# Optimization experiments

Measured on AMD Instinct MI355X. Metric: run time of the kernel, lower is better.

Reference implementation:

```python
import jax, jax.numpy as jnp
import numpy as np

TOP_K = 2
N_EXPERTS = 64
NEG_INF = -1e30  # stand-in for -inf; only used implicitly via sparse softmax


def setup_inputs() -> dict:
    key = jax.random.key(0)
    k1, k2, k3, k4 = jax.random.split(key, 4)
    n_embd, n_exp = 2048, N_EXPERTS
    B, S = 4, 4096
    scale = 1.0 / np.sqrt(n_embd)
    return {
        "x": jax.random.normal(k1, (B, S, n_embd), dtype=jnp.float32),
        "noise_eps": jax.random.normal(k2, (B, S, n_exp), dtype=jnp.float32),
        "W_route": jax.random.normal(k3, (n_embd, n_exp), dtype=jnp.float32) * scale,
        "b_route": jnp.zeros((n_exp,), dtype=jnp.float32),
        "W_noise": jax.random.normal(k4, (n_embd, n_exp), dtype=jnp.float32) * scale,
        "b_noise": jnp.zeros((n_exp,), dtype=jnp.float32),
    }


def reference(x, noise_eps, W_route, b_route, W_noise, b_noise):
    # r_act, noise_scale: [B, S, E]
    r_act = jnp.einsum("bsd,de->bse", x, W_route) + b_route
    noise_raw = jnp.einsum("bsd,de->bse", x, W_noise) + b_noise
    noisy = r_act + noise_eps * jax.nn.softplus(noise_raw)

    topk_logits, idx = jax.lax.top_k(noisy, TOP_K)  # [B, S, k]
    # softmax over a -inf-filled scatter == softmax over the top-k values,
    # scattered back with zeros elsewhere (exp(-inf) = 0)
    probs_k = jax.nn.softmax(topk_logits, axis=-1)  # [B, S, k]
    one_hot = jax.nn.one_hot(idx, N_EXPERTS, dtype=probs_k.dtype)  # [B, S, k, E]
    r_out = jnp.einsum("bsk,bske->bse", probs_k, one_hot)
    return r_out, idx
```

## Files before the change

### kernel.cpp

```cpp
#include <hip/hip_runtime.h>
#include <math.h>


typedef _Float16 f16;
typedef _Float16 f16x4 __attribute__((ext_vector_type(4)));
typedef _Float16 f16x8 __attribute__((ext_vector_type(8)));
typedef float    f32x4 __attribute__((ext_vector_type(4)));

#define NEMBD 2048
#define NEXP  64
#define BM    64
#define BK    32
#define NCH   (NEMBD / BK)
#define XP    40
#define WP    40
#define WSCALE 64.0f
#define INV_WSCALE 0.015625f

union F4H8 { float4 f; f16x8 h; };

__global__ __launch_bounds__(256) void build_wt(
    const float* __restrict__ Wr, const float* __restrict__ Wn,
    f16* __restrict__ wt_hi, f16* __restrict__ wt_lo)
{
    __shared__ float ws[BK][129];
    const int c = blockIdx.x, t = threadIdx.x;
    const int k0 = c * BK;
    {
        const int k  = t >> 3;
        const int n8 = (t & 7) << 3;
        const float* s0 = Wr + (size_t)(k0 + k) * NEXP + n8;
        const float* s1 = Wn + (size_t)(k0 + k) * NEXP + n8;
        #pragma unroll
        for (int j = 0; j < 8; ++j) ws[k][n8 + j] = s0[j];
        #pragma unroll
        for (int j = 0; j < 8; ++j) ws[k][64 + n8 + j] = s1[j];
    }
    __syncthreads();
    {
        const int n  = t >> 1;
        const int kh = (t & 1) << 4;
        f16x8 hv0, hv1, lv0, lv1;
        #pragma unroll
        for (int j = 0; j < 8; ++j) {
            const float v = ws[kh + j][n] * WSCALE;
            const f16 h = (f16)v;
            hv0[j] = h; lv0[j] = (f16)(v - (float)h);
        }
        #pragma unroll
        for (int j = 0; j < 8; ++j) {
            const float v = ws[kh + 8 + j][n] * WSCALE;
            const f16 h = (f16)v;
            hv1[j] = h; lv1[j] = (f16)(v - (float)h);
        }
        const size_t base = ((size_t)c * 128 + n) * 32 + kh;
        *(f16x8*)(wt_hi + base)     = hv0;
        *(f16x8*)(wt_hi + base + 8) = hv1;
        *(f16x8*)(wt_lo + base)     = lv0;
        *(f16x8*)(wt_lo + base + 8) = lv1;
    }
}

__global__ __launch_bounds__(512, 2) void router_fused(
    const float* __restrict__ x, const float* __restrict__ eps,
    const f16* __restrict__ wt_hi, const f16* __restrict__ wt_lo,
    const float* __restrict__ br, const float* __restrict__ bn,
    float* __restrict__ out_r, float* __restrict__ out_idx)
{
    __shared__ __align__(16) float smem_f[15360];
    f16* XH = (f16*)smem_f;
    f16* XL = XH + 2 * 64 * XP;
    f16* WH = XL + 2 * 64 * XP;
    f16* WL = WH + 2 * 128 * WP;
    float* LG = smem_f;
    float* TK = smem_f + 128 * 65;

    const int tid  = threadIdx.x;
    const int lane = tid & 63;
    const int w    = tid >> 6;
    const int wr   = w & 1, wc = w >> 1;
    const int m0   = blockIdx.x * BM;

    const int sxm = tid >> 3;
    const int sxk = (tid & 7) << 2;
    const float* xsrc = x + (size_t)(m0 + sxm) * NEMBD + sxk;
    const int xoff = sxm * XP + sxk;
    const int woff = (tid >> 2) * WP + ((tid & 3) << 3);

    const int arow0 = wr * 32 + (lane & 15);
    const int bcol0 = wc * 32 + (lane & 15);
    const int kgrp  = (lane >> 4) << 3;

    f32x4 acc[2][2];
    #pragma unroll
    for (int i = 0; i < 2; ++i)
        #pragma unroll
        for (int j = 0; j < 2; ++j)
            acc[i][j] = (f32x4){0.f, 0.f, 0.f, 0.f};

    {
        const float4 xv = *(const float4*)(xsrc);
        F4H8 whv, wlv;
        whv.f = *(const float4*)(wt_hi + (size_t)tid * 8);
        wlv.f = *(const float4*)(wt_lo + (size_t)tid * 8);
        f16x4 hv, lv;
        hv[0] = (f16)xv.x; lv[0] = (f16)(xv.x - (float)hv[0]);
        hv[1] = (f16)xv.y; lv[1] = (f16)(xv.y - (float)hv[1]);
        hv[2] = (f16)xv.z; lv[2] = (f16)(xv.z - (float)hv[2]);
        hv[3] = (f16)xv.w; lv[3] = (f16)(xv.w - (float)hv[3]);
        *(f16x4*)(XH + xoff) = hv;
        *(f16x4*)(XL + xoff) = lv;
        *(f16x8*)(WH + woff) = whv.h;
        *(f16x8*)(WL + woff) = wlv.h;
    }
    __syncthreads();

    for (int c = 0; c < NCH; ++c) {
        const int buf = c & 1;
        float4 nx; F4H8 nwh, nwl;
        const bool pf = (c + 1 < NCH);
        if (pf) {
            nx    = *(const float4*)(xsrc + (c + 1) * BK);
            nwh.f = *(const float4*)(wt_hi + (size_t)(c + 1) * 4096 + (size_t)tid * 8);
            nwl.f = *(const float4*)(wt_lo + (size_t)(c + 1) * 4096 + (size_t)tid * 8);
        }
        const f16* xh = XH + buf * 2560;
        const f16* xl = XL + buf * 2560;
        const f16* wh = WH + buf * 5120;
        const f16* wl = WL + buf * 5120;
        f16x8 ah[2], al[2], bh[2], bl[2];
        #pragma unroll
        for (int f = 0; f < 2; ++f) {
            ah[f] = *(const f16x8*)(xh + (arow0 + f * 16) * XP + kgrp);
            al[f] = *(const f16x8*)(xl + (arow0 + f * 16) * XP + kgrp);
            bh[f] = *(const f16x8*)(wh + (bcol0 + f * 16) * WP + kgrp);
            bl[f] = *(const f16x8*)(wl + (bcol0 + f * 16) * WP + kgrp);
        }
        #pragma unroll
        for (int i = 0; i < 2; ++i)
            #pragma unroll
            for (int j = 0; j < 2; ++j) {
                acc[i][j] = __builtin_amdgcn_mfma_f32_16x16x32_f16(ah[i], bh[j], acc[i][j], 0, 0, 0);
                acc[i][j] = __builtin_amdgcn_mfma_f32_16x16x32_f16(al[i], bh[j], acc[i][j], 0, 0, 0);
                acc[i][j] = __builtin_amdgcn_mfma_f32_16x16x32_f16(ah[i], bl[j], acc[i][j], 0, 0, 0);
            }
        if (pf) {
            const int nb = buf ^ 1;
            f16x4 hv, lv;
            hv[0] = (f16)nx.x; lv[0] = (f16)(nx.x - (float)hv[0]);
            hv[1] = (f16)nx.y; lv[1] = (f16)(nx.y - (float)hv[1]);
            hv[2] = (f16)nx.z; lv[2] = (f16)(nx.z - (float)hv[2]);
            hv[3] = (f16)nx.w; lv[3] = (f16)(nx.w - (float)hv[3]);
            *(f16x4*)(XH + nb * 2560 + xoff) = hv;
            *(f16x4*)(XL + nb * 2560 + xoff) = lv;
            *(f16x8*)(WH + nb * 5120 + woff) = nwh.h;
            *(f16x8*)(WL + nb * 5120 + woff) = nwl.h;
        }
        __syncthreads();
    }

    #pragma unroll
    for (int i = 0; i < 2; ++i) {
        const int tok = wr * 32 + i * 16 + ((lane >> 4) << 2);
        #pragma unroll
        for (int j = 0; j < 2; ++j) {
            const int col = wc * 32 + j * 16 + (lane & 15);
            const float bias = (col < NEXP) ? br[col] : bn[col - NEXP];
            #pragma unroll
            for (int r = 0; r < 4; ++r)
                LG[col * 65 + tok + r] = acc[i][j][r] * INV_WSCALE + bias;
        }
    }
    __syncthreads();

    if (tid < BM) {
        const int t = tid;
        const float* ep = eps + (size_t)(m0 + t) * NEXP;
        float v1 = -1e30f, v2 = -1e30f;
        int i1 = 0, i2 = 0;
        for (int e = 0; e < NEXP; ++e) {
            const float r  = LG[e * 65 + t];
            const float nr = LG[(NEXP + e) * 65 + t];
            const float sp = fmaxf(nr, 0.f) + log1pf(expf(-fabsf(nr)));
            const float noisy = fmaf(ep[e], sp, r);
            if (noisy > v1) { v2 = v1; i2 = i1; v1 = noisy; i1 = e; }
            else if (noisy > v2) { v2 = noisy; i2 = e; }
        }
        const float e2 = expf(v2 - v1);
        const float p1 = 1.f / (1.f + e2);
        TK[0 * 64 + t] = p1;
        TK[1 * 64 + t] = e2 * p1;
        TK[2 * 64 + t] = (float)i1;
        TK[3 * 64 + t] = (float)i2;
    }
    __syncthreads();

    {
        const int t  = tid >> 3;
        const int c8 = (tid & 7) << 3;
        const float p1 = TK[0 * 64 + t], p2 = TK[1 * 64 + t];
        const int i1 = (int)TK[2 * 64 + t], i2 = (int)TK[3 * 64 + t];
        float buf[8];
        #pragma unroll
        for (int j = 0; j < 8; ++j) {
            const int e = c8 + j;
            buf[j] = (e == i1) ? p1 : (e == i2) ? p2 : 0.f;
        }
        float* dst = out_r + (size_t)(m0 + t) * NEXP + c8;
        *(float4*)(dst + 0) = *(float4*)(buf + 0);
        *(float4*)(dst + 4) = *(float4*)(buf + 4);
    }
    if (tid < BM) {
        float2 v = make_float2(TK[2 * 64 + tid], TK[3 * 64 + tid]);
        *(float2*)(out_idx + (size_t)(m0 + tid) * 2) = v;
    }
}

__global__ __launch_bounds__(256) void router_fused_f32(
    const float* __restrict__ x, const float* __restrict__ eps,
    const float* __restrict__ Wr, const float* __restrict__ br,
    const float* __restrict__ Wn, const float* __restrict__ bn,
    float* __restrict__ out_r, float* __restrict__ out_idx)
{
    __shared__ float xs[BK][BM];
    __shared__ float ws2[BK][128];
    __shared__ float lg[128][BM];
    __shared__ float tk[4][BM];
    const int tid = threadIdx.x;
    const int tx = tid & 15, ty = tid >> 4;
    const int m0 = blockIdx.x * BM;
    float acc[4][8];
    #pragma unroll
    for (int i = 0; i < 4; ++i)
        #pragma unroll
        for (int j = 0; j < 8; ++j) acc[i][j] = 0.f;
    for (int kc = 0; kc < NEMBD; kc += BK) {
        {
            const int tm = tid >> 2, kk = (tid & 3) << 3;
            const float* src = x + (size_t)(m0 + tm) * NEMBD + kc + kk;
            const float4 a = *(const float4*)(src);
            const float4 b = *(const float4*)(src + 4);
            xs[kk+0][tm]=a.x; xs[kk+1][tm]=a.y; xs[kk+2][tm]=a.z; xs[kk+3][tm]=a.w;
            xs[kk+4][tm]=b.x; xs[kk+5][tm]=b.y; xs[kk+6][tm]=b.z; xs[kk+7][tm]=b.w;
        }
        {
            const int kr = tid >> 3, q = tid & 7;
            const float* src = (q < 4)
                ? (Wr + (size_t)(kc + kr) * NEXP + (q << 4))
                : (Wn + (size_t)(kc + kr) * NEXP + ((q - 4) << 4));
            float* dst = &ws2[kr][q << 4];
            #pragma unroll
            for (int j = 0; j < 16; ++j) dst[j] = src[j];
        }
        __syncthreads();
        #pragma unroll
        for (int k = 0; k < BK; ++k) {
            const float4 xv = *(const float4*)&xs[k][ty << 2];
            const float4 wa = *(const float4*)&ws2[k][tx << 3];
            const float4 wb = *(const float4*)&ws2[k][(tx << 3) + 4];
            const float xr[4] = {xv.x, xv.y, xv.z, xv.w};
            const float wcx[8] = {wa.x, wa.y, wa.z, wa.w, wb.x, wb.y, wb.z, wb.w};
            #pragma unroll
            for (int i = 0; i < 4; ++i)
                #pragma unroll
                for (int j = 0; j < 8; ++j)
                    acc[i][j] = fmaf(xr[i], wcx[j], acc[i][j]);
        }
        __syncthreads();
    }
    {
        const int n0 = tx << 3;
        #pragma unroll
        for (int j = 0; j < 8; ++j) {
            const int n = n0 + j;
            const float b = (n < NEXP) ? br[n] : bn[n - NEXP];
            #pragma unroll
            for (int i = 0; i < 4; ++i)
                lg[n][(ty << 2) + i] = acc[i][j] + b;
        }
    }
    __syncthreads();
    if (tid < BM) {
        const int t = tid;
        const float* ep = eps + (size_t)(m0 + t) * NEXP;
        float v1 = -1e30f, v2 = -1e30f; int i1 = 0, i2 = 0;
        for (int e = 0; e < NEXP; ++e) {
            const float r = lg[e][t], nr = lg[NEXP + e][t];
            const float sp = fmaxf(nr, 0.f) + log1pf(expf(-fabsf(nr)));
            const float noisy = fmaf(ep[e], sp, r);
            if (noisy > v1) { v2=v1; i2=i1; v1=noisy; i1=e; }
            else if (noisy > v2) { v2=noisy; i2=e; }
        }
        const float e2 = expf(v2 - v1);
        const float p1 = 1.f / (1.f + e2);
        tk[0][t]=p1; tk[1][t]=e2*p1; tk[2][t]=(float)i1; tk[3][t]=(float)i2;
    }
    __syncthreads();
    {
        const int t = tid >> 2, c = tid & 3;
        const float p1 = tk[0][t], p2 = tk[1][t];
        const int i1 = (int)tk[2][t], i2 = (int)tk[3][t];
        float buf[16];
        #pragma unroll
        for (int j = 0; j < 16; ++j) {
            const int e = (c << 4) + j;
            buf[j] = (e == i1) ? p1 : (e == i2) ? p2 : 0.f;
        }
        float* dst = out_r + (size_t)(m0 + t) * NEXP + (c << 4);
        *(float4*)(dst+0)=*(float4*)(buf+0); *(float4*)(dst+4)=*(float4*)(buf+4);
        *(float4*)(dst+8)=*(float4*)(buf+8); *(float4*)(dst+12)=*(float4*)(buf+12);
    }
    if (tid < BM) {
        float2 v = make_float2(tk[2][tid], tk[3][tid]);
        *(float2*)(out_idx + (size_t)(m0 + tid) * 2) = v;
    }
}

extern "C" void kernel_launch(void* const* d_in, const int* in_sizes, int n_in,
                              void* d_out, int out_size, void* d_ws, size_t ws_size,
                              hipStream_t stream) {
    const float* x  = (const float*)d_in[0];
    const float* ep = (const float*)d_in[1];
    const float* Wr = (const float*)d_in[2];
    const float* br = (const float*)d_in[3];
    const float* Wn = (const float*)d_in[4];
    const float* bn = (const float*)d_in[5];

    const int T = in_sizes[1] / NEXP;
    float* out_r   = (float*)d_out;
    float* out_idx = (float*)d_out + (size_t)T * NEXP;

    const size_t limb = (size_t)128 * NEMBD * sizeof(f16);
    if (ws_size >= 2 * limb) {
        f16* wt_hi = (f16*)d_ws;
        f16* wt_lo = wt_hi + (size_t)128 * NEMBD;
        build_wt<<<NCH, 256, 0, stream>>>(Wr, Wn, wt_hi, wt_lo);
        router_fused<<<T / BM, 512, 0, stream>>>(
            x, ep, wt_hi, wt_lo, br, bn, out_r, out_idx);
    } else {
        router_fused_f32<<<T / BM, 256, 0, stream>>>(
            x, ep, Wr, br, Wn, bn, out_r, out_idx);
    }
}
```

Measured before the change: 76.12 us.

## Halve token tile, read split weights straight into registers, two-lane top-k

New measurement: 86.74 us. 13.9% more time.

```diff
diff --git a/kernel.cpp b/kernel.cpp
--- a/kernel.cpp
+++ b/kernel.cpp
@@ -3,17 +3,16 @@
 
 
 typedef _Float16 f16;
-typedef _Float16 f16x4 __attribute__((ext_vector_type(4)));
+typedef _Float16 f16x2 __attribute__((ext_vector_type(2)));
 typedef _Float16 f16x8 __attribute__((ext_vector_type(8)));
 typedef float    f32x4 __attribute__((ext_vector_type(4)));
 
 #define NEMBD 2048
 #define NEXP  64
-#define BM    64
+#define BM    32
 #define BK    32
-#define NCH   (NEMBD / BK)
+#define NCH   64
 #define XP    40
-#define WP    40
 #define WSCALE 64.0f
 #define INV_WSCALE 0.015625f
 
@@ -61,19 +60,69 @@
     }
 }
 
-__global__ __launch_bounds__(512, 2) void router_fused(
+__device__ __forceinline__ void wsplit2(float a, float b, f16x2& hi, f16x2& lo) {
+    const f16 h0 = (f16)a, h1 = (f16)b;
+    hi = (f16x2){h0, h1};
+    lo = (f16x2){(f16)(a - (float)h0), (f16)(b - (float)h1)};
+}
+
+__device__ __forceinline__ void loadB(const f16* wt_hi, const f16* wt_lo,
+    int c, int boff0, int boff1,
+    f16x8& bh0, f16x8& bh1, f16x8& bl0, f16x8& bl1)
+{
+    const size_t cb = (size_t)c * 4096;
+    F4H8 u0, u1, u2, u3;
+    u0.f = *(const float4*)(wt_hi + cb + boff0);
+    u1.f = *(const float4*)(wt_hi + cb + boff1);
+    u2.f = *(const float4*)(wt_lo + cb + boff0);
+    u3.f = *(const float4*)(wt_lo + cb + boff1);
+    bh0 = u0.h; bh1 = u1.h; bl0 = u2.h; bl1 = u3.h;
+}
+
+__device__ __forceinline__ void step(
+    int c, bool doX, bool doB, bool doW,
+    const float* xsrc, const f16* wt_hi, const f16* wt_lo,
+    int boff0, int boff1, int aoff, int xwoff,
+    const f16* XHr, const f16* XLr, f16* XHw, f16* XLw,
+    float2& xsI, const float2& xsW,
+    f16x8& biH0, f16x8& biH1, f16x8& biL0, f16x8& biL1,
+    const f16x8& buH0, const f16x8& buH1, const f16x8& buL0, const f16x8& buL1,
+    f32x4& acc0, f32x4& acc1)
+{
+    if (doX) xsI = *(const float2*)(xsrc + (c + 2) * BK);
+    if (doB) loadB(wt_hi, wt_lo, c + 1, boff0, boff1, biH0, biH1, biL0, biL1);
+    const f16x8 ah = *(const f16x8*)(XHr + aoff);
+    const f16x8 al = *(const f16x8*)(XLr + aoff);
+    acc0 = __builtin_amdgcn_mfma_f32_16x16x32_f16(ah, buH0, acc0, 0, 0, 0);
+    acc0 = __builtin_amdgcn_mfma_f32_16x16x32_f16(al, buH0, acc0, 0, 0, 0);
+    acc0 = __builtin_amdgcn_mfma_f32_16x16x32_f16(ah, buL0, acc0, 0, 0, 0);
+    acc1 = __builtin_amdgcn_mfma_f32_16x16x32_f16(ah, buH1, acc1, 0, 0, 0);
+    acc1 = __builtin_amdgcn_mfma_f32_16x16x32_f16(al, buH1, acc1, 0, 0, 0);
+    acc1 = __builtin_amdgcn_mfma_f32_16x16x32_f16(ah, buL1, acc1, 0, 0, 0);
+    if (doW) {
+        f16x2 hi, lo;
+        wsplit2(xsW.x, xsW.y, hi, lo);
+        *(f16x2*)(XHw + xwoff) = hi;
+        *(f16x2*)(XLw + xwoff) = lo;
+    }
+    asm volatile("s_waitcnt lgkmcnt(0)" ::: "memory");
+    __builtin_amdgcn_s_barrier();
+    asm volatile("" ::: "memory");
+}
+
+__global__ __launch_bounds__(512, 4) void router_fused2(
     const float* __restrict__ x, const float* __restrict__ eps,
     const f16* __restrict__ wt_hi, const f16* __restrict__ wt_lo,
     const float* __restrict__ br, const float* __restrict__ bn,
     float* __restrict__ out_r, float* __restrict__ out_idx)
 {
-    __shared__ __align__(16) float smem_f[15360];
-    f16* XH = (f16*)smem_f;
-    f16* XL = XH + 2 * 64 * XP;
-    f16* WH = XL + 2 * 64 * XP;
-    f16* WL = WH + 2 * 128 * WP;
-    float* LG = smem_f;
-    float* TK = smem_f + 128 * 65;
+    __shared__ __align__(16) float smem[4352];
+    f16* XH0 = (f16*)smem;
+    f16* XH1 = XH0 + 1280;
+    f16* XL0 = XH0 + 2560;
+    f16* XL1 = XH0 + 3840;
+    float* LG = smem;
+    float* TK = smem + 128 * 33;
 
     const int tid  = threadIdx.x;
     const int lane = tid & 63;
@@ -81,137 +130,119 @@
     const int wr   = w & 1, wc = w >> 1;
     const int m0   = blockIdx.x * BM;
 
-    const int sxm = tid >> 3;
-    const int sxk = (tid & 7) << 2;
-    const float* xsrc = x + (size_t)(m0 + sxm) * NEMBD + sxk;
-    const int xoff = sxm * XP + sxk;
-    const int woff = (tid >> 2) * WP + ((tid & 3) << 3);
-
-    const int arow0 = wr * 32 + (lane & 15);
-    const int bcol0 = wc * 32 + (lane & 15);
-    const int kgrp  = (lane >> 4) << 3;
-
-    f32x4 acc[2][2];
+    const int sxr = tid >> 4;
+    const int sxk = (tid & 15) << 1;
+    const float* xsrc = x + (size_t)(m0 + sxr) * NEMBD + sxk;
+    const int xwoff = sxr * XP + sxk;
+
+    const int arow = wr * 16 + (lane & 15);
+    const int kgrp = (lane >> 4) << 3;
+    const int aoff = arow * XP + kgrp;
+
+    const int bcol  = wc * 32 + (lane & 15);
+    const int boff0 = bcol * 32 + kgrp;
+    const int boff1 = (bcol + 16) * 32 + kgrp;
+
+    f32x4 acc0 = {0.f, 0.f, 0.f, 0.f}, acc1 = {0.f, 0.f, 0.f, 0.f};
+    float2 xs0, xs1;
+    f16x8 b0h0, b0h1, b0l0, b0l1, b1h0, b1h1, b1l0, b1l1;
+
+    {
+        const float2 x0 = *(const float2*)(xsrc);
+        f16x2 hi, lo;
+        wsplit2(x0.x, x0.y, hi, lo);
+        *(f16x2*)(XH0 + xwoff) = hi;
+        *(f16x2*)(XL0 + xwoff) = lo;
+        xs1 = *(const float2*)(xsrc + BK);
+        loadB(wt_hi, wt_lo, 0, boff0, boff1, b1h0, b1h1, b1l0, b1l1);
+        asm volatile("s_waitcnt lgkmcnt(0)" ::: "memory");
+        __builtin_amdgcn_s_barrier();
+        asm volatile("" ::: "memory");
+    }
+
+    for (int c = 0; c < NCH - 2; c += 2) {
+        step(c,     true, true, true, xsrc, wt_hi, wt_lo, boff0, boff1, aoff, xwoff,
+             XH0, XL0, XH1, XL1, xs0, xs1,
+             b0h0, b0h1, b0l0, b0l1, b1h0, b1h1, b1l0, b1l1, acc0, acc1);
+        step(c + 1, true, true, true, xsrc, wt_hi, wt_lo, boff0, boff1, aoff, xwoff,
+             XH1, XL1, XH0, XL0, xs1, xs0,
+             b1h0, b1h1, b1l0, b1l1, b0h0, b0h1, b0l0, b0l1, acc0, acc1);
+    }
+    step(62, false, true, true, xsrc, wt_hi, wt_lo, boff0, boff1, aoff, xwoff,
+         XH0, XL0, XH1, XL1, xs0, xs1,
+         b0h0, b0h1, b0l0, b0l1, b1h0, b1h1, b1l0, b1l1, acc0, acc1);
+    step(63, false, false, false, xsrc, wt_hi, wt_lo, boff0, boff1, aoff, xwoff,
+         XH1, XL1, XH0, XL0, xs1, xs0,
+         b1h0, b1h1, b1l0, b1l1, b0h0, b0h1, b0l0, b0l1, acc0, acc1);
+
     #pragma unroll
-    for (int i = 0; i < 2; ++i)
-        #pragma unroll
-        for (int j = 0; j < 2; ++j)
-            acc[i][j] = (f32x4){0.f, 0.f, 0.f, 0.f};
-
-    {
-        const float4 xv = *(const float4*)(xsrc);
-        F4H8 whv, wlv;
-        whv.f = *(const float4*)(wt_hi + (size_t)tid * 8);
-        wlv.f = *(const float4*)(wt_lo + (size_t)tid * 8);
-        f16x4 hv, lv;
-        hv[0] = (f16)xv.x; lv[0] = (f16)(xv.x - (float)hv[0]);
-        hv[1] = (f16)xv.y; lv[1] = (f16)(xv.y - (float)hv[1]);
-        hv[2] = (f16)xv.z; lv[2] = (f16)(xv.z - (float)hv[2]);
-        hv[3] = (f16)xv.w; lv[3] = (f16)(xv.w - (float)hv[3]);
-        *(f16x4*)(XH + xoff) = hv;
-        *(f16x4*)(XL + xoff) = lv;
-        *(f16x8*)(WH + woff) = whv.h;
-        *(f16x8*)(WL + woff) = wlv.h;
-    }
-    __syncthreads();
-
-    for (int c = 0; c < NCH; ++c) {
-        const int buf = c & 1;
-        float4 nx; F4H8 nwh, nwl;
-        const bool pf = (c + 1 < NCH);
-        if (pf) {
-            nx    = *(const float4*)(xsrc + (c + 1) * BK);
-            nwh.f = *(const float4*)(wt_hi + (size_t)(c + 1) * 4096 + (size_t)tid * 8);
-            nwl.f = *(const float4*)(wt_lo + (size_t)(c + 1) * 4096 + (size_t)tid * 8);
-        }
-        const f16* xh = XH + buf * 2560;
-        const f16* xl = XL + buf * 2560;
-        const f16* wh = WH + buf * 5120;
-        const f16* wl = WL + buf * 5120;
-        f16x8 ah[2], al[2], bh[2], bl[2];
-        #pragma unroll
-        for (int f = 0; f < 2; ++f) {
-            ah[f] = *(const f16x8*)(xh + (arow0 + f * 16) * XP + kgrp);
-            al[f] = *(const f16x8*)(xl + (arow0 + f * 16) * XP + kgrp);
-            bh[f] = *(const f16x8*)(wh + (bcol0 + f * 16) * WP + kgrp);
-            bl[f] = *(const f16x8*)(wl + (bcol0 + f * 16) * WP + kgrp);
-        }
-        #pragma unroll
-        for (int i = 0; i < 2; ++i)
-            #pragma unroll
-            for (int j = 0; j < 2; ++j) {
-                acc[i][j] = __builtin_amdgcn_mfma_f32_16x16x32_f16(ah[i], bh[j], acc[i][j], 0, 0, 0);
-                acc[i][j] = __builtin_amdgcn_mfma_f32_16x16x32_f16(al[i], bh[j], acc[i][j], 0, 0, 0);
-                acc[i][j] = __builtin_amdgcn_mfma_f32_16x16x32_f16(ah[i], bl[j], acc[i][j], 0, 0, 0);
-            }
-        if (pf) {
-            const int nb = buf ^ 1;
-            f16x4 hv, lv;
-            hv[0] = (f16)nx.x; lv[0] = (f16)(nx.x - (float)hv[0]);
-            hv[1] = (f16)nx.y; lv[1] = (f16)(nx.y - (float)hv[1]);
-            hv[2] = (f16)nx.z; lv[2] = (f16)(nx.z - (float)hv[2]);
-            hv[3] = (f16)nx.w; lv[3] = (f16)(nx.w - (float)hv[3]);
-            *(f16x4*)(XH + nb * 2560 + xoff) = hv;
-            *(f16x4*)(XL + nb * 2560 + xoff) = lv;
-            *(f16x8*)(WH + nb * 5120 + woff) = nwh.h;
-            *(f16x8*)(WL + nb * 5120 + woff) = nwl.h;
-        }
-        __syncthreads();
-    }
-
-    #pragma unroll
-    for (int i = 0; i < 2; ++i) {
-        const int tok = wr * 32 + i * 16 + ((lane >> 4) << 2);
-        #pragma unroll
-        for (int j = 0; j < 2; ++j) {
-            const int col = wc * 32 + j * 16 + (lane & 15);
-            const float bias = (col < NEXP) ? br[col] : bn[col - NEXP];
-            #pragma unroll
-            for (int r = 0; r < 4; ++r)
-                LG[col * 65 + tok + r] = acc[i][j][r] * INV_WSCALE + bias;
-        }
-    }
-    __syncthreads();
-
-    if (tid < BM) {
-        const int t = tid;
+    for (int j = 0; j < 2; ++j) {
+        const int col = wc * 32 + j * 16 + (lane & 15);
+        const float bias = (col < NEXP) ? br[col] : bn[col - NEXP];
+        const int tokb = wr * 16 + ((lane >> 4) << 2);
+        const f32x4 a = j ? acc1 : acc0;
+        #pragma unroll
+        for (int r = 0; r < 4; ++r)
+            LG[col * 33 + tokb + r] = a[r] * INV_WSCALE + bias;
+    }
+    __syncthreads();
+
+    if (tid < 64) {
+        const int t = tid >> 1;
+        const int h = tid & 1;
         const float* ep = eps + (size_t)(m0 + t) * NEXP;
         float v1 = -1e30f, v2 = -1e30f;
         int i1 = 0, i2 = 0;
-        for (int e = 0; e < NEXP; ++e) {
-            const float r  = LG[e * 65 + t];
-            const float nr = LG[(NEXP + e) * 65 + t];
+        for (int j = 0; j < 32; ++j) {
+            const int e = h * 32 + j;
+            const float r  = LG[e * 33 + t];
+            const float nr = LG[(NEXP + e) * 33 + t];
             const float sp = fmaxf(nr, 0.f) + log1pf(expf(-fabsf(nr)));
             const float noisy = fmaf(ep[e], sp, r);
             if (noisy > v1) { v2 = v1; i2 = i1; v1 = noisy; i1 = e; }
             else if (noisy > v2) { v2 = noisy; i2 = e; }
         }
-        const float e2 = expf(v2 - v1);
-        const float p1 = 1.f / (1.f + e2);
-        TK[0 * 64 + t] = p1;
-        TK[1 * 64 + t] = e2 * p1;
-        TK[2 * 64 + t] = (float)i1;
-        TK[3 * 64 + t] = (float)i2;
-    }
-    __syncthreads();
-
-    {
-        const int t  = tid >> 3;
-        const int c8 = (tid & 7) << 3;
-        const float p1 = TK[0 * 64 + t], p2 = TK[1 * 64 + t];
-        const int i1 = (int)TK[2 * 64 + t], i2 = (int)TK[3 * 64 + t];
-        float buf[8];
-        #pragma unroll
-        for (int j = 0; j < 8; ++j) {
-            const int e = c8 + j;
-            buf[j] = (e == i1) ? p1 : (e == i2) ? p2 : 0.f;
-        }
-        float* dst = out_r + (size_t)(m0 + t) * NEXP + c8;
-        *(float4*)(dst + 0) = *(float4*)(buf + 0);
-        *(float4*)(dst + 4) = *(float4*)(buf + 4);
+        const float ov1 = __shfl_xor(v1, 1);
+        const float ov2 = __shfl_xor(v2, 1);
+        const int   oi1 = __shfl_xor(i1, 1);
+        const int   oi2 = __shfl_xor(i2, 1);
+        float a1, a2, bb1, bb2; int ai1, ai2, bj1, bj2;
+        if (h) { a1 = ov1; a2 = ov2; ai1 = oi1; ai2 = oi2; bb1 = v1; bb2 = v2; bj1 = i1; bj2 = i2; }
+        else   { a1 = v1;  a2 = v2;  ai1 = i1;  ai2 = i2;  bb1 = ov1; bb2 = ov2; bj1 = oi1; bj2 = oi2; }
+        float t1, t2; int ti1, ti2;
+        if (bb1 > a1) {
+            t1 = bb1; ti1 = bj1;
+            if (a1 >= bb2) { t2 = a1; ti2 = ai1; } else { t2 = bb2; ti2 = bj2; }
+        } else {
+            t1 = a1; ti1 = ai1;
+            if (bb1 > a2) { t2 = bb1; ti2 = bj1; } else { t2 = a2; ti2 = ai2; }
+        }
+        if (h == 0) {
+            const float e2 = expf(t2 - t1);
+            const float p1 = 1.f / (1.f + e2);
+            TK[0 * 32 + t] = p1;
+            TK[1 * 32 + t] = e2 * p1;
+            TK[2 * 32 + t] = (float)ti1;
+            TK[3 * 32 + t] = (float)ti2;
+        }
+    }
+    __syncthreads();
+
+    {
+        const int t  = tid >> 4;
+        const int c4 = (tid & 15) << 2;
+        const float p1 = TK[t], p2 = TK[32 + t];
+        const int i1 = (int)TK[64 + t], i2 = (int)TK[96 + t];
+        float buf[4];
+        #pragma unroll
+        for (int jj = 0; jj < 4; ++jj) {
+            const int e = c4 + jj;
+            buf[jj] = (e == i1) ? p1 : (e == i2) ? p2 : 0.f;
+        }
+        *(float4*)(out_r + (size_t)(m0 + t) * NEXP + c4) = *(float4*)buf;
     }
     if (tid < BM) {
-        float2 v = make_float2(TK[2 * 64 + tid], TK[3 * 64 + tid]);
+        float2 v = make_float2(TK[64 + tid], TK[96 + tid]);
         *(float2*)(out_idx + (size_t)(m0 + tid) * 2) = v;
     }
 }
@@ -222,13 +253,13 @@
     const float* __restrict__ Wn, const float* __restrict__ bn,
     float* __restrict__ out_r, float* __restrict__ out_idx)
 {
-    __shared__ float xs[BK][BM];
+    __shared__ float xs[BK][64];
     __shared__ float ws2[BK][128];
-    __shared__ float lg[128][BM];
-    __shared__ float tk[4][BM];
+    __shared__ float lg[128][64];
+    __shared__ float tk[4][64];
     const int tid = threadIdx.x;
     const int tx = tid & 15, ty = tid >> 4;
-    const int m0 = blockIdx.x * BM;
+    const int m0 = blockIdx.x * 64;
     float acc[4][8];
     #pragma unroll
     for (int i = 0; i < 4; ++i)
@@ -280,7 +311,7 @@
         }
     }
     __syncthreads();
-    if (tid < BM) {
+    if (tid < 64) {
         const int t = tid;
         const float* ep = eps + (size_t)(m0 + t) * NEXP;
         float v1 = -1e30f, v2 = -1e30f; int i1 = 0, i2 = 0;
@@ -310,7 +341,7 @@
         *(float4*)(dst+0)=*(float4*)(buf+0); *(float4*)(dst+4)=*(float4*)(buf+4);
         *(float4*)(dst+8)=*(float4*)(buf+8); *(float4*)(dst+12)=*(float4*)(buf+12);
     }
-    if (tid < BM) {
+    if (tid < 64) {
         float2 v = make_float2(tk[2][tid], tk[3][tid]);
         *(float2*)(out_idx + (size_t)(m0 + tid) * 2) = v;
     }
@@ -335,10 +366,10 @@
         f16* wt_hi = (f16*)d_ws;
         f16* wt_lo = wt_hi + (size_t)128 * NEMBD;
         build_wt<<<NCH, 256, 0, stream>>>(Wr, Wn, wt_hi, wt_lo);
-        router_fused<<<T / BM, 512, 0, stream>>>(
+        router_fused2<<<T / BM, 512, 0, stream>>>(
             x, ep, wt_hi, wt_lo, br, bn, out_r, out_idx);
     } else {
-        router_fused_f32<<<T / BM, 256, 0, stream>>>(
+        router_fused_f32<<<T / 64, 256, 0, stream>>>(
             x, ep, Wr, br, Wn, bn, out_r, out_idx);
     }
 }
```
